# Optimization experiments

Measured on AMD Instinct MI355X. Metric: run time of the kernel, lower is better.

Reference implementation:

```python
import jax, jax.numpy as jnp
import numpy as np

DIM = 1024
NHEADS = 16
DIM_HEAD = 64
HIDDEN = NHEADS * DIM_HEAD  # 1024


def _xavier(key, fan_in, fan_out):
    limit = np.sqrt(6.0 / (fan_in + fan_out))
    return jax.random.uniform(key, (fan_in, fan_out), jnp.float32, -limit, limit)


def setup_inputs() -> dict:
    key = jax.random.key(0)
    kq, k1, k2, k3 = jax.random.split(key, 4)
    q = jax.random.normal(kq, (2, 2048, DIM), jnp.float32)
    Wq = _xavier(k1, DIM, HIDDEN)
    bq = jnp.zeros((HIDDEN,), jnp.float32)
    Wkv = _xavier(k2, DIM, 2 * HIDDEN)
    bkv = jnp.zeros((2 * HIDDEN,), jnp.float32)
    Wo = _xavier(k3, HIDDEN, DIM)
    bo = jnp.zeros((DIM,), jnp.float32)
    return {"q": q, "Wq": Wq, "bq": bq, "Wkv": Wkv, "bkv": bkv, "Wo": Wo, "bo": bo}


def reference(q, Wq, bq, Wkv, bkv, Wo, bo):
    scale = DIM_HEAD ** (-0.5)
    query = q @ Wq + bq                      # [b, s, hidden]
    kv = q @ Wkv + bkv                       # self-attention: kv from q
    key_, value = jnp.split(kv, 2, axis=-1)  # [b, s, hidden] each
    b, s, _ = query.shape
    query = query.reshape(b, s, NHEADS, DIM_HEAD)
    key_ = key_.reshape(b, s, NHEADS, DIM_HEAD)
    value = value.reshape(b, s, NHEADS, DIM_HEAD)
    scores = jnp.einsum('bqhd,bkhd->bhqk', query, key_) * scale
    attn = jax.nn.softmax(scores, axis=-1)
    out = jnp.einsum('bhqk,bkhd->bqhd', attn, value)
    out = out.reshape(b, s, HIDDEN)
    return out @ Wo + bo
```

## Files before the change

kernel.cpp:

```cpp
#include <hip/hip_runtime.h>

#define DIM 1024
#define NHEADS 16
#define DH 64
#define BATCH 2
#define SEQ 2048

typedef float f32x4 __attribute__((ext_vector_type(4)));
typedef short s16x8 __attribute__((ext_vector_type(8)));
typedef short s16x4 __attribute__((ext_vector_type(4)));

__device__ __forceinline__ short f2bf(float f) {
    union { float f; unsigned u; } v; v.f = f;
    unsigned r = v.u + 0x7fffu + ((v.u >> 16) & 1u);
    return (short)(r >> 16);
}

#if defined(__has_builtin)
#if __has_builtin(__builtin_amdgcn_cvt_pk_bf16_f32)
#define HAVE_PK_BF16 1
#endif
#endif
__device__ __forceinline__ unsigned f2bf_pk(float a, float b) {
#ifdef HAVE_PK_BF16
    typedef __bf16 bf16x2_t __attribute__((ext_vector_type(2)));
    bf16x2_t r = __builtin_amdgcn_cvt_pk_bf16_f32(a, b);
    return __builtin_bit_cast(unsigned, r);
#else
    return ((unsigned)(unsigned short)f2bf(b) << 16) | (unsigned short)f2bf(a);
#endif
}
__device__ __forceinline__ s16x4 pk4(float a, float b, float c, float d) {
    union { unsigned u[2]; s16x4 v; } x;
    x.u[0] = f2bf_pk(a, b); x.u[1] = f2bf_pk(c, d);
    return x.v;
}

#if defined(__has_builtin)
#if __has_builtin(__builtin_amdgcn_exp2f)
#define EXP2(x) __builtin_amdgcn_exp2f(x)
#endif
#endif
#ifndef EXP2
#define EXP2(x) exp2f(x)
#endif

__device__ __forceinline__ void gld16(const void* g, void* l) {
    __builtin_amdgcn_global_load_lds(
        (const __attribute__((address_space(1))) void*)g,
        (__attribute__((address_space(3))) void*)l, 16, 0, 0);
}

__global__ __launch_bounds__(256) void prep_kernel(
    const float* __restrict__ X, short* __restrict__ Y,
    const float* __restrict__ Wq, const float* __restrict__ Wkv,
    const float* __restrict__ Wo, short* __restrict__ WT)
{
    const int t = threadIdx.x;
    if (blockIdx.x < 2048) {
        const int i = (blockIdx.x * 256 + t) * 8;
        float4 a = *(const float4*)(X + i);
        float4 b = *(const float4*)(X + i + 4);
        union { unsigned u[4]; s16x8 v; } o;
        o.u[0] = f2bf_pk(a.x, a.y); o.u[1] = f2bf_pk(a.z, a.w);
        o.u[2] = f2bf_pk(b.x, b.y); o.u[3] = f2bf_pk(b.z, b.w);
        *(s16x8*)(Y + i) = o.v;
    } else {
        const int i2 = blockIdx.x - 2048;
        const int bx = i2 & 63, by = i2 >> 6;
        const int ng = bx * 64 + (t & 63);
        const int k0 = (by * 4 + (t >> 6)) * 8;
        const float* W; int n, N;
        if (ng < 1024)      { W = Wq;  n = ng;        N = 1024; }
        else if (ng < 3072) { W = Wkv; n = ng - 1024; N = 2048; }
        else                { W = Wo;  n = ng - 3072; N = 1024; }
        float v[8];
#pragma unroll
        for (int j = 0; j < 8; ++j) v[j] = W[(size_t)(k0 + j) * N + n];
        union { unsigned u[4]; s16x8 s; } o;
        o.u[0] = f2bf_pk(v[0], v[1]); o.u[1] = f2bf_pk(v[2], v[3]);
        o.u[2] = f2bf_pk(v[4], v[5]); o.u[3] = f2bf_pk(v[6], v[7]);
        *(s16x8*)&WT[(size_t)ng * 1024 + k0] = o.s;
    }
}

__global__ __launch_bounds__(256) void transpose_v_kernel(
    const short* __restrict__ QKV, short* __restrict__ VtG)
{
    const int t = threadIdx.x;
    const int tok0 = blockIdx.x * 64;
    const int h = blockIdx.y, b = blockIdx.z;
    __shared__ short L[64 * 72];
    const short* src = QKV + (size_t)(b * SEQ + tok0) * 3072 + 2048 + h * 64;
#pragma unroll
    for (int p = 0; p < 2; ++p) {
        int r = p * 32 + (t >> 3);
        *(s16x8*)&L[r * 72 + (t & 7) * 8] = *(const s16x8*)(src + (size_t)r * 3072 + (t & 7) * 8);
    }
    __syncthreads();
    short* dst = VtG + (size_t)(b * NHEADS + h) * 64 * SEQ + tok0;
#pragma unroll
    for (int p = 0; p < 2; ++p) {
        int u = p * 256 + t;
        int dv = u >> 3, c = (u & 7) * 8;
        s16x8 o;
#pragma unroll
        for (int j = 0; j < 8; ++j) o[j] = L[(c + j) * 72 + dv];
        *(s16x8*)(dst + (size_t)dv * SEQ + c) = o;
    }
}

template<int TM, bool OUT_BF16>
__global__ __launch_bounds__(256) void gemm_mfma_kernel(
    const short* __restrict__ A, const short* __restrict__ Bt,
    const float* __restrict__ bias0, const float* __restrict__ bias1, int nsplit,
    float s0, float s1, void* __restrict__ C, int M, int N)
{
    const int K = 1024;
    constexpr int NI = (TM == 128) ? 4 : 2;
    __shared__ short As[TM * 32];
    __shared__ short Bs[128 * 32];

    const int t    = threadIdx.x;
    const int wave = t >> 6;
    const int lane = t & 63;
    const int col  = lane & 15;
    const int quad = lane >> 4;
    const int m0 = blockIdx.y * TM;
    const int n0 = blockIdx.x * 128;
    const int wroff = (TM == 128) ? (wave >> 1) * 64 : 0;
    const int wcoff = (TM == 128) ? (wave & 1) * 64 : wave * 32;

    f32x4 acc[4][NI];
#pragma unroll
    for (int mi = 0; mi < 4; ++mi)
#pragma unroll
        for (int ni = 0; ni < NI; ++ni) acc[mi][ni] = (f32x4){0.f, 0.f, 0.f, 0.f};

    constexpr int RPW = TM / 4;
    const int ldrowA = wave * RPW + (lane >> 2);
    const int ldrowB = wave * 32  + (lane >> 2);
    const int ldcol  = (lane & 3) * 8;
    const short* Ag = A  + (size_t)(m0 + ldrowA) * K + ldcol;
    const short* Bg = Bt + (size_t)(n0 + ldrowB) * K + ldcol;
    short* AsW = &As[wave * RPW * 32];
    short* BsW = &Bs[wave * 1024];

    for (int k0 = 0; k0 < K; k0 += 32) {
        __syncthreads();
        gld16(Ag + k0, AsW);
        if (TM == 128) gld16(Ag + 16 * K + k0, AsW + 512);
        gld16(Bg + k0,          BsW);
        gld16(Bg + 16 * K + k0, BsW + 512);
        __syncthreads();

        s16x8 aA[4], bB[NI];
#pragma unroll
        for (int mi = 0; mi < 4; ++mi)
            aA[mi] = *(const s16x8*)&As[(wroff + 16 * mi + col) * 32 + quad * 8];
#pragma unroll
        for (int ni = 0; ni < NI; ++ni)
            bB[ni] = *(const s16x8*)&Bs[(wcoff + 16 * ni + col) * 32 + quad * 8];
#pragma unroll
        for (int mi = 0; mi < 4; ++mi)
#pragma unroll
            for (int ni = 0; ni < NI; ++ni)
                acc[mi][ni] = __builtin_amdgcn_mfma_f32_16x16x32_bf16(aA[mi], bB[ni], acc[mi][ni], 0, 0, 0);
    }

    float bias_v[NI], scale_v[NI];
#pragma unroll
    for (int ni = 0; ni < NI; ++ni) {
        int nb = n0 + wcoff + 16 * ni + col;
        bias_v[ni]  = (nb < nsplit) ? bias0[nb] : bias1[nb - nsplit];
        scale_v[ni] = (nb < nsplit) ? s0 : s1;
    }

#pragma unroll
    for (int mi = 0; mi < 4; ++mi)
#pragma unroll
        for (int ni = 0; ni < NI; ++ni)
#pragma unroll
            for (int r = 0; r < 4; ++r) {
                const int gm = m0 + wroff + 16 * mi + quad * 4 + r;
                const int gn = n0 + wcoff + 16 * ni + col;
                float v = (acc[mi][ni][r] + bias_v[ni]) * scale_v[ni];
                if (OUT_BF16) ((short*)C)[(size_t)gm * N + gn] = f2bf(v);
                else          ((float*)C)[(size_t)gm * N + gn] = v;
            }
}

__global__ __launch_bounds__(512, 4) void attn_v11_kernel(
    const short* __restrict__ QKV,
    const short* __restrict__ VtG,
    short* __restrict__ O)
{
    const int L = blockIdx.x + 16 * blockIdx.y + 256 * blockIdx.z;
    const int xcd = L & 7, idx = L >> 3;
    const int pair = xcd * 4 + (idx >> 4);
    const int qt = idx & 15;
    const int h  = pair & 15;
    const int b  = pair >> 4;
    const int t  = threadIdx.x;
    const int wave = t >> 6;
    const int lane = t & 63;
    const int col  = lane & 15;
    const int quad = lane >> 4;
    const int wq = wave & 3;
    const int kh = wave >> 2;

    __shared__ __align__(16) short Lds[19456];
    short* Ks  = Lds;
    short* Vt  = Lds + 4608;
    short* PsW = Lds + 9216 + wave * (32 * 40);

    const short* Qg = QKV + (size_t)(b * SEQ + qt * 128) * 3072 + h * DH;
    const short* Kg = QKV + (size_t)(b * SEQ) * 3072 + 1024 + h * DH;
    const short* VtRow = VtG + (size_t)(b * NHEADS + h) * 64 * SEQ;

    s16x8 aQ[2][2];
#pragma unroll
    for (int tq = 0; tq < 2; ++tq)
#pragma unroll
        for (int kq = 0; kq < 2; ++kq)
            aQ[tq][kq] = *(const s16x8*)(Qg + (size_t)(wq * 32 + 16 * tq + col) * 3072 + kq * 32 + quad * 8);

    f32x4 oa[4][2];
    float lsum[2] = {0.f, 0.f};
#pragma unroll
    for (int td = 0; td < 4; ++td)
#pragma unroll
        for (int tq = 0; tq < 2; ++tq) oa[td][tq] = (f32x4){0.f, 0.f, 0.f, 0.f};

    const int srow = t >> 3;
    const int sc8  = (t & 7) * 8;
    const short* KgS  = Kg + (size_t)srow * 3072 + sc8;
    const short* VtgS = VtRow + (size_t)srow * SEQ + sc8;
    s16x8 kx = *(const s16x8*)KgS;
    s16x8 vx = *(const s16x8*)VtgS;

    for (int kt = 0; kt < SEQ / 64; ++kt) {
        __syncthreads();
        *(s16x8*)&Ks[srow * 72 + sc8] = kx;
        *(s16x8*)&Vt[srow * 72 + sc8] = vx;
        __syncthreads();
        {
            int nt = (kt + 1 < SEQ / 64) ? kt + 1 : kt;
            kx = *(const s16x8*)(KgS + (size_t)nt * 64 * 3072);
            vx = *(const s16x8*)(VtgS + (size_t)nt * 64);
        }

        s16x8 aK[2][2];
#pragma unroll
        for (int tk = 0; tk < 2; ++tk)
#pragma unroll
            for (int kq = 0; kq < 2; ++kq)
                aK[tk][kq] = *(const s16x8*)&Ks[(kh * 32 + 16 * tk + col) * 72 + kq * 32 + quad * 8];
        f32x4 st[2][2];
        __builtin_amdgcn_s_setprio(1);
#pragma unroll
        for (int tk = 0; tk < 2; ++tk)
#pragma unroll
            for (int tq = 0; tq < 2; ++tq) {
                f32x4 a = (f32x4){0.f, 0.f, 0.f, 0.f};
                a = __builtin_amdgcn_mfma_f32_16x16x32_bf16(aK[tk][0], aQ[tq][0], a, 0, 0, 0);
                a = __builtin_amdgcn_mfma_f32_16x16x32_bf16(aK[tk][1], aQ[tq][1], a, 0, 0, 0);
                st[tk][tq] = a;
            }
        __builtin_amdgcn_s_setprio(0);

#pragma unroll
        for (int tk = 0; tk < 2; ++tk)
#pragma unroll
            for (int tq = 0; tq < 2; ++tq) {
                float p0 = EXP2(st[tk][tq][0]);
                float p1 = EXP2(st[tk][tq][1]);
                float p2 = EXP2(st[tk][tq][2]);
                float p3 = EXP2(st[tk][tq][3]);
                lsum[tq] += (p0 + p1) + (p2 + p3);
                *(s16x4*)&PsW[(16 * tq + col) * 40 + 16 * tk + quad * 4] = pk4(p0, p1, p2, p3);
            }
        asm volatile("s_waitcnt lgkmcnt(0)" ::: "memory");

        s16x8 bP[2];
#pragma unroll
        for (int tq = 0; tq < 2; ++tq)
            bP[tq] = *(const s16x8*)&PsW[(16 * tq + col) * 40 + quad * 8];
        __builtin_amdgcn_s_setprio(1);
#pragma unroll
        for (int td = 0; td < 4; ++td) {
            const int dv = 16 * td + col;
            s16x8 aV = *(const s16x8*)&Vt[dv * 72 + kh * 32 + quad * 8];
#pragma unroll
            for (int tq = 0; tq < 2; ++tq)
                oa[td][tq] = __builtin_amdgcn_mfma_f32_16x16x32_bf16(aV, bP[tq], oa[td][tq], 0, 0, 0);
        }
        __builtin_amdgcn_s_setprio(0);
    }

#pragma unroll
    for (int tq = 0; tq < 2; ++tq) {
        lsum[tq] += __shfl_xor(lsum[tq], 16);
        lsum[tq] += __shfl_xor(lsum[tq], 32);
    }

    __syncthreads();
    float* red  = (float*)Lds;
    float* redl = red + 4 * 64 * 36;
    if (wave >= 4) {
        const int slot = wave & 3;
#pragma unroll
        for (int td = 0; td < 4; ++td)
#pragma unroll
            for (int tq = 0; tq < 2; ++tq)
#pragma unroll
                for (int r = 0; r < 4; ++r)
                    red[slot * 2304 + (16 * td + quad * 4 + r) * 36 + 16 * tq + col] = oa[td][tq][r];
        if (quad == 0)
#pragma unroll
            for (int tq = 0; tq < 2; ++tq)
                redl[slot * 32 + 16 * tq + col] = lsum[tq];
    }
    __syncthreads();

    if (wave < 4) {
        const int slot = wq;
#pragma unroll
        for (int td = 0; td < 4; ++td)
#pragma unroll
            for (int tq = 0; tq < 2; ++tq)
#pragma unroll
                for (int r = 0; r < 4; ++r)
                    oa[td][tq][r] += red[slot * 2304 + (16 * td + quad * 4 + r) * 36 + 16 * tq + col];
        float inv[2];
#pragma unroll
        for (int tq = 0; tq < 2; ++tq) {
            lsum[tq] += redl[slot * 32 + 16 * tq + col];
            inv[tq] = 1.f / lsum[tq];
        }
        short* Og = O + (size_t)(b * SEQ + qt * 128 + wq * 32) * DIM + h * DH;
#pragma unroll
        for (int td = 0; td < 4; ++td)
#pragma unroll
            for (int tq = 0; tq < 2; ++tq)
                *(s16x4*)(Og + (size_t)(16 * tq + col) * DIM + 16 * td + quad * 4) =
                    pk4(oa[td][tq][0] * inv[tq], oa[td][tq][1] * inv[tq],
                        oa[td][tq][2] * inv[tq], oa[td][tq][3] * inv[tq]);
    }
}

extern "C" void kernel_launch(void* const* d_in, const int* in_sizes, int n_in,
                              void* d_out, int out_size, void* d_ws, size_t ws_size,
                              hipStream_t stream)
{
    const float* q   = (const float*)d_in[0];
    const float* Wq  = (const float*)d_in[1];
    const float* bq  = (const float*)d_in[2];
    const float* Wkv = (const float*)d_in[3];
    const float* bkv = (const float*)d_in[4];
    const float* Wo  = (const float*)d_in[5];
    const float* bo  = (const float*)d_in[6];
    float* out = (float*)d_out;

    const int M = BATCH * SEQ;

    short* qb     = (short*)d_ws;
    short* WT     = qb     + (size_t)M * DIM;
    short* QKVbuf = WT     + (size_t)4096 * DIM;
    short* AObuf  = QKVbuf + (size_t)M * 3 * DIM;
    short* VtG    = (short*)d_out;

    const float QSCALE = 0.18033688011112042f;

    prep_kernel<<<4096, 256, 0, stream>>>(q, qb, Wq, Wkv, Wo, WT);

    gemm_mfma_kernel<128, true><<<dim3(3 * DIM / 128, M / 128), 256, 0, stream>>>(
        qb, WT, bq, bkv, DIM, QSCALE, 1.0f, QKVbuf, M, 3 * DIM);
    transpose_v_kernel<<<dim3(SEQ / 64, NHEADS, BATCH), 256, 0, stream>>>(QKVbuf, VtG);
    attn_v11_kernel<<<dim3(SEQ / 128, NHEADS, BATCH), 512, 0, stream>>>(QKVbuf, VtG, AObuf);
    gemm_mfma_kernel<64, false><<<dim3(DIM / 128, M / 64), 256, 0, stream>>>(
        AObuf, WT + (size_t)3072 * 1024, bo, bo, 1 << 30, 1.0f, 1.0f, out, M, DIM);
}
```

Before: 191.3 us.

## Double-buffer K/V tiles in LDS and pass P through lane shuffles

The attention kernel now alternates between two LDS buffers for the K and V^T tiles, so each iteration needs one barrier instead of two. The softmax probabilities are packed to bf16 in registers and rearranged into the MFMA B-operand layout with cross-lane shuffles, replacing the per-wave LDS scratch write, wait and read-back. This trades LDS traffic and a barrier for extra shuffle and select instructions. LDS use drops slightly, which may help occupancy.

```diff
diff --git a/kernel.cpp b/kernel.cpp
--- a/kernel.cpp
+++ b/kernel.cpp
@@ -190,7 +190,7 @@
             }
 }
 
-__global__ __launch_bounds__(512, 4) void attn_v11_kernel(
+__global__ __launch_bounds__(512, 4) void attn_v13_kernel(
     const short* __restrict__ QKV,
     const short* __restrict__ VtG,
     short* __restrict__ O)
@@ -209,10 +209,9 @@
     const int wq = wave & 3;
     const int kh = wave >> 2;
 
-    __shared__ __align__(16) short Lds[19456];
-    short* Ks  = Lds;
-    short* Vt  = Lds + 4608;
-    short* PsW = Lds + 9216 + wave * (32 * 40);
+    __shared__ __align__(16) short Lds[18688];
+    short* KsB = Lds;
+    short* VtB = Lds + 2 * 64 * 72;
 
     const short* Qg = QKV + (size_t)(b * SEQ + qt * 128) * 3072 + h * DH;
     const short* Kg = QKV + (size_t)(b * SEQ) * 3072 + 1024 + h * DH;
@@ -239,23 +238,27 @@
     s16x8 kx = *(const s16x8*)KgS;
     s16x8 vx = *(const s16x8*)VtgS;
 
+    const int shfl_s0 = col + 32 * (quad & 1);
+    const int shfl_s1 = shfl_s0 + 16;
+    const bool loquad = (quad < 2);
+
     for (int kt = 0; kt < SEQ / 64; ++kt) {
-        __syncthreads();
-        *(s16x8*)&Ks[srow * 72 + sc8] = kx;
-        *(s16x8*)&Vt[srow * 72 + sc8] = vx;
-        __syncthreads();
+        const int cur = kt & 1;
+        *(s16x8*)&KsB[cur * 4608 + srow * 72 + sc8] = kx;
+        *(s16x8*)&VtB[cur * 4608 + srow * 72 + sc8] = vx;
         {
             int nt = (kt + 1 < SEQ / 64) ? kt + 1 : kt;
             kx = *(const s16x8*)(KgS + (size_t)nt * 64 * 3072);
             vx = *(const s16x8*)(VtgS + (size_t)nt * 64);
         }
+        __syncthreads();
 
         s16x8 aK[2][2];
 #pragma unroll
         for (int tk = 0; tk < 2; ++tk)
 #pragma unroll
             for (int kq = 0; kq < 2; ++kq)
-                aK[tk][kq] = *(const s16x8*)&Ks[(kh * 32 + 16 * tk + col) * 72 + kq * 32 + quad * 8];
+                aK[tk][kq] = *(const s16x8*)&KsB[cur * 4608 + (kh * 32 + 16 * tk + col) * 72 + kq * 32 + quad * 8];
         f32x4 st[2][2];
         __builtin_amdgcn_s_setprio(1);
 #pragma unroll
@@ -269,6 +272,7 @@
             }
         __builtin_amdgcn_s_setprio(0);
 
+        unsigned pk[2][2][2];
 #pragma unroll
         for (int tk = 0; tk < 2; ++tk)
 #pragma unroll
@@ -278,19 +282,31 @@
                 float p2 = EXP2(st[tk][tq][2]);
                 float p3 = EXP2(st[tk][tq][3]);
                 lsum[tq] += (p0 + p1) + (p2 + p3);
-                *(s16x4*)&PsW[(16 * tq + col) * 40 + 16 * tk + quad * 4] = pk4(p0, p1, p2, p3);
+                pk[tk][tq][0] = f2bf_pk(p0, p1);
+                pk[tk][tq][1] = f2bf_pk(p2, p3);
             }
-        asm volatile("s_waitcnt lgkmcnt(0)" ::: "memory");
 
         s16x8 bP[2];
 #pragma unroll
-        for (int tq = 0; tq < 2; ++tq)
-            bP[tq] = *(const s16x8*)&PsW[(16 * tq + col) * 40 + quad * 8];
+        for (int tq = 0; tq < 2; ++tq) {
+            union { unsigned u[4]; s16x8 v; } bp;
+            unsigned a0, b0;
+            a0 = __shfl((int)pk[0][tq][0], shfl_s0); b0 = __shfl((int)pk[1][tq][0], shfl_s0);
+            bp.u[0] = loquad ? a0 : b0;
+            a0 = __shfl((int)pk[0][tq][1], shfl_s0); b0 = __shfl((int)pk[1][tq][1], shfl_s0);
+            bp.u[1] = loquad ? a0 : b0;
+            a0 = __shfl((int)pk[0][tq][0], shfl_s1); b0 = __shfl((int)pk[1][tq][0], shfl_s1);
+            bp.u[2] = loquad ? a0 : b0;
+            a0 = __shfl((int)pk[0][tq][1], shfl_s1); b0 = __shfl((int)pk[1][tq][1], shfl_s1);
+            bp.u[3] = loquad ? a0 : b0;
+            bP[tq] = bp.v;
+        }
+
         __builtin_amdgcn_s_setprio(1);
 #pragma unroll
         for (int td = 0; td < 4; ++td) {
             const int dv = 16 * td + col;
-            s16x8 aV = *(const s16x8*)&Vt[dv * 72 + kh * 32 + quad * 8];
+            s16x8 aV = *(const s16x8*)&VtB[cur * 4608 + dv * 72 + kh * 32 + quad * 8];
 #pragma unroll
             for (int tq = 0; tq < 2; ++tq)
                 oa[td][tq] = __builtin_amdgcn_mfma_f32_16x16x32_bf16(aV, bP[tq], oa[td][tq], 0, 0, 0);
@@ -377,7 +393,7 @@
     gemm_mfma_kernel<128, true><<<dim3(3 * DIM / 128, M / 128), 256, 0, stream>>>(
         qb, WT, bq, bkv, DIM, QSCALE, 1.0f, QKVbuf, M, 3 * DIM);
     transpose_v_kernel<<<dim3(SEQ / 64, NHEADS, BATCH), 256, 0, stream>>>(QKVbuf, VtG);
-    attn_v11_kernel<<<dim3(SEQ / 128, NHEADS, BATCH), 512, 0, stream>>>(QKVbuf, VtG, AObuf);
+    attn_v13_kernel<<<dim3(SEQ / 128, NHEADS, BATCH), 512, 0, stream>>>(QKVbuf, VtG, AObuf);
     gemm_mfma_kernel<64, false><<<dim3(DIM / 128, M / 64), 256, 0, stream>>>(
         AObuf, WT + (size_t)3072 * 1024, bo, bo, 1 << 30, 1.0f, 1.0f, out, M, DIM);
 }
```

Result: slower. 200.9 us (+5.0%).

## Load V fragments straight to registers and double-buffer K tiles in LDS

Applied to the files above, without the earlier changes.

V fragments for the PV MFMA are now read directly from global memory into registers and prefetched one tile ahead, so V no longer passes through LDS. K tiles are double-buffered in LDS, which drops one of the two barriers per iteration. This cuts LDS traffic and synchronisation in exchange for more VGPRs and uncoalesced-ish global reads of V per wave, which may raise register pressure under launch_bounds(512,4). The PsW region still sits at offset 9216, so the second K buffer (4608..9215) fits in the space freed by V.

```diff
diff --git a/kernel.cpp b/kernel.cpp
--- a/kernel.cpp
+++ b/kernel.cpp
@@ -190,7 +190,7 @@
             }
 }
 
-__global__ __launch_bounds__(512, 4) void attn_v11_kernel(
+__global__ __launch_bounds__(512, 4) void attn_v14_kernel(
     const short* __restrict__ QKV,
     const short* __restrict__ VtG,
     short* __restrict__ O)
@@ -210,9 +210,8 @@
     const int kh = wave >> 2;
 
     __shared__ __align__(16) short Lds[19456];
-    short* Ks  = Lds;
-    short* Vt  = Lds + 4608;
-    short* PsW = Lds + 9216 + wave * (32 * 40);
+    short* KsB = Lds;
+    short* PsW = Lds + 9216 + wave * 1280;
 
     const short* Qg = QKV + (size_t)(b * SEQ + qt * 128) * 3072 + h * DH;
     const short* Kg = QKV + (size_t)(b * SEQ) * 3072 + 1024 + h * DH;
@@ -234,28 +233,30 @@
 
     const int srow = t >> 3;
     const int sc8  = (t & 7) * 8;
-    const short* KgS  = Kg + (size_t)srow * 3072 + sc8;
-    const short* VtgS = VtRow + (size_t)srow * SEQ + sc8;
+    const short* KgS = Kg + (size_t)srow * 3072 + sc8;
     s16x8 kx = *(const s16x8*)KgS;
-    s16x8 vx = *(const s16x8*)VtgS;
+
+    const short* VtL = VtRow + (size_t)col * SEQ + kh * 32 + quad * 8;
+    s16x8 vG[4];
+#pragma unroll
+    for (int td = 0; td < 4; ++td)
+        vG[td] = *(const s16x8*)(VtL + (size_t)td * 16 * SEQ);
 
     for (int kt = 0; kt < SEQ / 64; ++kt) {
-        __syncthreads();
-        *(s16x8*)&Ks[srow * 72 + sc8] = kx;
-        *(s16x8*)&Vt[srow * 72 + sc8] = vx;
-        __syncthreads();
+        const int cur = kt & 1;
+        *(s16x8*)&KsB[cur * 4608 + srow * 72 + sc8] = kx;
         {
             int nt = (kt + 1 < SEQ / 64) ? kt + 1 : kt;
             kx = *(const s16x8*)(KgS + (size_t)nt * 64 * 3072);
-            vx = *(const s16x8*)(VtgS + (size_t)nt * 64);
         }
+        __syncthreads();
 
         s16x8 aK[2][2];
 #pragma unroll
         for (int tk = 0; tk < 2; ++tk)
 #pragma unroll
             for (int kq = 0; kq < 2; ++kq)
-                aK[tk][kq] = *(const s16x8*)&Ks[(kh * 32 + 16 * tk + col) * 72 + kq * 32 + quad * 8];
+                aK[tk][kq] = *(const s16x8*)&KsB[cur * 4608 + (kh * 32 + 16 * tk + col) * 72 + kq * 32 + quad * 8];
         f32x4 st[2][2];
         __builtin_amdgcn_s_setprio(1);
 #pragma unroll
@@ -288,14 +289,18 @@
             bP[tq] = *(const s16x8*)&PsW[(16 * tq + col) * 40 + quad * 8];
         __builtin_amdgcn_s_setprio(1);
 #pragma unroll
-        for (int td = 0; td < 4; ++td) {
-            const int dv = 16 * td + col;
-            s16x8 aV = *(const s16x8*)&Vt[dv * 72 + kh * 32 + quad * 8];
-#pragma unroll
-            for (int tq = 0; tq < 2; ++tq)
-                oa[td][tq] = __builtin_amdgcn_mfma_f32_16x16x32_bf16(aV, bP[tq], oa[td][tq], 0, 0, 0);
+        for (int td = 0; td < 4; ++td)
+#pragma unroll
+            for (int tq = 0; tq < 2; ++tq)
+                oa[td][tq] = __builtin_amdgcn_mfma_f32_16x16x32_bf16(vG[td], bP[tq], oa[td][tq], 0, 0, 0);
+        __builtin_amdgcn_s_setprio(0);
+
+        {
+            int nt = (kt + 1 < SEQ / 64) ? kt + 1 : kt;
+#pragma unroll
+            for (int td = 0; td < 4; ++td)
+                vG[td] = *(const s16x8*)(VtL + (size_t)td * 16 * SEQ + (size_t)nt * 64);
         }
-        __builtin_amdgcn_s_setprio(0);
     }
 
 #pragma unroll
@@ -377,7 +382,7 @@
     gemm_mfma_kernel<128, true><<<dim3(3 * DIM / 128, M / 128), 256, 0, stream>>>(
         qb, WT, bq, bkv, DIM, QSCALE, 1.0f, QKVbuf, M, 3 * DIM);
     transpose_v_kernel<<<dim3(SEQ / 64, NHEADS, BATCH), 256, 0, stream>>>(QKVbuf, VtG);
-    attn_v11_kernel<<<dim3(SEQ / 128, NHEADS, BATCH), 512, 0, stream>>>(QKVbuf, VtG, AObuf);
+    attn_v14_kernel<<<dim3(SEQ / 128, NHEADS, BATCH), 512, 0, stream>>>(QKVbuf, VtG, AObuf);
     gemm_mfma_kernel<64, false><<<dim3(DIM / 128, M / 64), 256, 0, stream>>>(
         AObuf, WT + (size_t)3072 * 1024, bo, bo, 1 << 30, 1.0f, 1.0f, out, M, DIM);
 }
```

After: 212.3 us. +11.0%, slower.

## Split attention keys into two halves with a merge kernel; swizzle QKV GEMM blocks

Applied to the files above, without the earlier changes.

The attention kernel now splits the key sequence into two halves, so twice as many blocks run over shorter loops. Each half writes bf16 partial outputs and per-row softmax sums, and a new merge kernel combines them with weights based on those sums. The partial results reuse workspace and output buffers whose earlier contents are no longer needed. The QKV GEMM also remaps block indices so tiles are grouped per XCD for better cache locality. The cost is an extra kernel launch, extra memory traffic for the partials, and an added bf16 rounding step before the merge.

```diff
diff --git a/kernel.cpp b/kernel.cpp
--- a/kernel.cpp
+++ b/kernel.cpp
@@ -14,6 +14,9 @@
     union { float f; unsigned u; } v; v.f = f;
     unsigned r = v.u + 0x7fffu + ((v.u >> 16) & 1u);
     return (short)(r >> 16);
+}
+__device__ __forceinline__ float bf2f(short s) {
+    union { unsigned u; float f; } x; x.u = (unsigned)(unsigned short)s << 16; return x.f;
 }
 
 #if defined(__has_builtin)
@@ -126,8 +129,16 @@
     const int lane = t & 63;
     const int col  = lane & 15;
     const int quad = lane >> 4;
-    const int m0 = blockIdx.y * TM;
-    const int n0 = blockIdx.x * 128;
+
+    int bx = blockIdx.x, by = blockIdx.y;
+    if (TM == 128) {
+        const int Lb = bx + 24 * by;
+        const int x = Lb & 7, i = Lb >> 3;
+        by = (x & 3) * 8 + (i & 7);
+        bx = (x >> 2) * 12 + (i >> 3);
+    }
+    const int m0 = by * TM;
+    const int n0 = bx * 128;
     const int wroff = (TM == 128) ? (wave >> 1) * 64 : 0;
     const int wcoff = (TM == 128) ? (wave & 1) * 64 : wave * 32;
 
@@ -190,17 +201,19 @@
             }
 }
 
-__global__ __launch_bounds__(512, 4) void attn_v11_kernel(
+__global__ __launch_bounds__(512, 4) void attn_v17_kernel(
     const short* __restrict__ QKV,
     const short* __restrict__ VtG,
-    short* __restrict__ O)
-{
-    const int L = blockIdx.x + 16 * blockIdx.y + 256 * blockIdx.z;
+    short* __restrict__ P0, short* __restrict__ P1,
+    float* __restrict__ Lsum)
+{
+    const int L = blockIdx.x;
     const int xcd = L & 7, idx = L >> 3;
-    const int pair = xcd * 4 + (idx >> 4);
-    const int qt = idx & 15;
-    const int h  = pair & 15;
-    const int b  = pair >> 4;
+    const int pair = xcd * 4 + (idx >> 5);
+    const int rem  = idx & 31;
+    const int qt   = rem & 15;
+    const int half = rem >> 4;
+    const int h = pair & 15, b = pair >> 4;
     const int t  = threadIdx.x;
     const int wave = t >> 6;
     const int lane = t & 63;
@@ -212,11 +225,11 @@
     __shared__ __align__(16) short Lds[19456];
     short* Ks  = Lds;
     short* Vt  = Lds + 4608;
-    short* PsW = Lds + 9216 + wave * (32 * 40);
+    short* PsW = Lds + 9216 + wave * 1280;
 
     const short* Qg = QKV + (size_t)(b * SEQ + qt * 128) * 3072 + h * DH;
-    const short* Kg = QKV + (size_t)(b * SEQ) * 3072 + 1024 + h * DH;
-    const short* VtRow = VtG + (size_t)(b * NHEADS + h) * 64 * SEQ;
+    const short* Kg = QKV + (size_t)(b * SEQ + half * 1024) * 3072 + 1024 + h * DH;
+    const short* VtRow = VtG + (size_t)pair * 64 * SEQ + half * 1024;
 
     s16x8 aQ[2][2];
 #pragma unroll
@@ -239,13 +252,13 @@
     s16x8 kx = *(const s16x8*)KgS;
     s16x8 vx = *(const s16x8*)VtgS;
 
-    for (int kt = 0; kt < SEQ / 64; ++kt) {
+    for (int kt = 0; kt < 16; ++kt) {
         __syncthreads();
         *(s16x8*)&Ks[srow * 72 + sc8] = kx;
         *(s16x8*)&Vt[srow * 72 + sc8] = vx;
         __syncthreads();
         {
-            int nt = (kt + 1 < SEQ / 64) ? kt + 1 : kt;
+            int nt = (kt + 1 < 16) ? kt + 1 : kt;
             kx = *(const s16x8*)(KgS + (size_t)nt * 64 * 3072);
             vx = *(const s16x8*)(VtgS + (size_t)nt * 64);
         }
@@ -338,7 +351,7 @@
             lsum[tq] += redl[slot * 32 + 16 * tq + col];
             inv[tq] = 1.f / lsum[tq];
         }
-        short* Og = O + (size_t)(b * SEQ + qt * 128 + wq * 32) * DIM + h * DH;
+        short* Og = (half ? P1 : P0) + (size_t)(b * SEQ + qt * 128 + wq * 32) * DIM + h * DH;
 #pragma unroll
         for (int td = 0; td < 4; ++td)
 #pragma unroll
@@ -346,7 +359,41 @@
                 *(s16x4*)(Og + (size_t)(16 * tq + col) * DIM + 16 * td + quad * 4) =
                     pk4(oa[td][tq][0] * inv[tq], oa[td][tq][1] * inv[tq],
                         oa[td][tq][2] * inv[tq], oa[td][tq][3] * inv[tq]);
-    }
+        if (quad == 0) {
+            float* Lp = Lsum + half * (32 * SEQ) + (size_t)pair * SEQ + qt * 128 + wq * 32;
+#pragma unroll
+            for (int tq = 0; tq < 2; ++tq)
+                Lp[16 * tq + col] = lsum[tq];
+        }
+    }
+}
+
+__global__ __launch_bounds__(256) void merge_kernel(
+    const short* __restrict__ P0, const short* __restrict__ P1,
+    const float* __restrict__ Lsum, short* __restrict__ O)
+{
+    const int bid = blockIdx.x;
+    const int t = threadIdx.x;
+    const int xcd = bid & 7, i = bid >> 3;
+    const int pair = xcd * 4 + (i >> 6);
+    const int chunk = i & 63;
+    const int tok = chunk * 32 + (t >> 3);
+    const int dv  = (t & 7) * 8;
+    const int b = pair >> 4, h = pair & 15;
+    const size_t off = (size_t)(b * SEQ + tok) * DIM + h * 64 + dv;
+    const int li = pair * SEQ + tok;
+    const float l0 = Lsum[li], l1 = Lsum[32 * SEQ + li];
+    const float inv = 1.f / (l0 + l1);
+    const float w0 = l0 * inv, w1 = l1 * inv;
+    s16x8 a = *(const s16x8*)(P0 + off);
+    s16x8 c = *(const s16x8*)(P1 + off);
+    float r[8];
+#pragma unroll
+    for (int j = 0; j < 8; ++j) r[j] = bf2f(a[j]) * w0 + bf2f(c[j]) * w1;
+    union { unsigned u[4]; s16x8 v; } o;
+    o.u[0] = f2bf_pk(r[0], r[1]); o.u[1] = f2bf_pk(r[2], r[3]);
+    o.u[2] = f2bf_pk(r[4], r[5]); o.u[3] = f2bf_pk(r[6], r[7]);
+    *(s16x8*)(O + off) = o.v;
 }
 
 extern "C" void kernel_launch(void* const* d_in, const int* in_sizes, int n_in,
@@ -369,6 +416,9 @@
     short* QKVbuf = WT     + (size_t)4096 * DIM;
     short* AObuf  = QKVbuf + (size_t)M * 3 * DIM;
     short* VtG    = (short*)d_out;
+    short* P0     = qb;
+    short* P1     = VtG + (size_t)4 * 1024 * 1024;
+    float* Lsum   = (float*)(WT + (size_t)1024 * 1024);
 
     const float QSCALE = 0.18033688011112042f;
 
@@ -377,7 +427,8 @@
     gemm_mfma_kernel<128, true><<<dim3(3 * DIM / 128, M / 128), 256, 0, stream>>>(
         qb, WT, bq, bkv, DIM, QSCALE, 1.0f, QKVbuf, M, 3 * DIM);
     transpose_v_kernel<<<dim3(SEQ / 64, NHEADS, BATCH), 256, 0, stream>>>(QKVbuf, VtG);
-    attn_v11_kernel<<<dim3(SEQ / 128, NHEADS, BATCH), 512, 0, stream>>>(QKVbuf, VtG, AObuf);
+    attn_v17_kernel<<<1024, 512, 0, stream>>>(QKVbuf, VtG, P0, P1, Lsum);
+    merge_kernel<<<2048, 256, 0, stream>>>(P0, P1, Lsum, AObuf);
     gemm_mfma_kernel<64, false><<<dim3(DIM / 128, M / 64), 256, 0, stream>>>(
         AObuf, WT + (size_t)3072 * 1024, bo, bo, 1 << 30, 1.0f, 1.0f, out, M, DIM);
 }
```

New measurement: 197.8 us. +3.4%, slower.
